# Kernel optimization log

Hardware: AMD Instinct MI355X
Metric: run time of the kernel (lower is better)

## Reference

```python
import jax, jax.numpy as jnp
import numpy as np

N, E, G = 20000, 320000, 128
HID, HEADS, LAYERS, IN = 128, 4, 2, 74
EPS = 1e-5


def setup_inputs() -> dict:
    key = jax.random.key(0)
    ks = jax.random.split(key, 10)
    h = jax.random.normal(ks[0], (N, IN), dtype=jnp.float32)
    src = jax.random.randint(ks[1], (E,), 0, N, dtype=jnp.int32)
    dst = jax.random.randint(ks[2], (E,), 0, N, dtype=jnp.int32)
    graph_ids = jnp.sort(jax.random.randint(ks[3], (N,), 0, G, dtype=jnp.int32))
    W0 = jax.random.normal(ks[4], (HEADS, IN, HID), dtype=jnp.float32) / np.sqrt(IN)
    Wr = jax.random.normal(ks[5], (LAYERS - 1, HEADS, HID, HID), dtype=jnp.float32) / np.sqrt(HID)
    att = jax.random.normal(ks[6], (LAYERS, HEADS, 2 * HID), dtype=jnp.float32) / np.sqrt(2 * HID)
    gamma = jnp.ones((LAYERS, HEADS, HID), dtype=jnp.float32)
    beta = jnp.zeros((LAYERS, HEADS, HID), dtype=jnp.float32)
    out_w = jax.random.normal(ks[7], (LAYERS, HID), dtype=jnp.float32) / np.sqrt(HID)
    out_b = jnp.zeros((LAYERS,), dtype=jnp.float32)
    return {"h": h, "src": src, "dst": dst, "graph_ids": graph_ids,
            "W0": W0, "Wr": Wr, "att": att, "gamma": gamma, "beta": beta,
            "out_w": out_w, "out_b": out_b}


def _gat_head(h, W, a, g, b, src, dst):
    # h: [N, F_in], W: [F_in, HID], a: [2*HID]
    z = h @ W                                  # [N, HID]
    zs, zd = z[src], z[dst]                    # [E, HID] gathers
    e = jax.nn.leaky_relu(zs @ a[:HID] + zd @ a[HID:])  # [E] edge logits
    # segment softmax over incoming edges of each dst node
    emax = jax.ops.segment_max(e, dst, num_segments=N)
    ex = jnp.exp(e - emax[dst])
    denom = jax.ops.segment_sum(ex, dst, num_segments=N)
    alpha = ex / denom[dst]
    hout = jax.ops.segment_sum(alpha[:, None] * zs, dst, num_segments=N)  # [N, HID]
    r = jax.nn.relu(hout)
    # BatchNorm1d (training-mode batch stats, biased variance)
    mean = r.mean(0)
    var = r.var(0)
    return g * (r - mean) / jnp.sqrt(var + EPS) + b


def reference(h, src, dst, graph_ids, W0, Wr, att, gamma, beta, out_w, out_b):
    heads = jax.vmap(_gat_head, in_axes=(None, 0, 0, 0, 0, None, None))
    x = h
    for j in range(LAYERS):
        W = W0 if j == 0 else Wr[j - 1]
        hs = heads(x, W, att[j], gamma[j], beta[j], src, dst)  # [HEADS, N, HID]
        hs = jnp.transpose(hs, (1, 0, 2))                       # [N, HEADS, HID]
        score = jax.nn.softmax(hs @ out_w[j] + out_b[j], axis=1)  # [N, HEADS]
        x = jnp.einsum('nh,nhd->nd', score, hs)                 # [N, HID]
    # dgl.mean_nodes: per-graph mean of node features
    counts = jax.ops.segment_sum(jnp.ones((N,), dtype=x.dtype), graph_ids, num_segments=G)
    sums = jax.ops.segment_sum(x, graph_ids, num_segments=G)
    return sums / jnp.maximum(counts, 1.0)[:, None]
```

## Files before the change

kernel.cpp:

```cpp
#include <hip/hip_runtime.h>
#include <hip/hip_bf16.h>

typedef unsigned short u16;
typedef unsigned int u32;
typedef __attribute__((ext_vector_type(8))) short bf16x8;
typedef __attribute__((ext_vector_type(4))) float f32x4;
typedef __attribute__((ext_vector_type(2))) float f32x2;

#define NN 20000
#define NE 320000
#define NG 128
#define HD 128
#define NH 4
#define KIN 74
#define KP0 96
#define BN_EPS 1e-5f
#define SCAN_B 20

__device__ __forceinline__ float bf2f(u16 v){ return __uint_as_float(((u32)v)<<16); }
__device__ __forceinline__ float bflo(u32 v){ return __uint_as_float(v<<16); }
__device__ __forceinline__ float bfhi(u32 v){ return __uint_as_float(v & 0xffff0000u); }
__device__ __forceinline__ u16 f2bf(float f){
    u32 u = __float_as_uint(f);
    return (u16)((u + 0x7fffu + ((u>>16)&1u)) >> 16);
}
__device__ __forceinline__ u32 pack2(float a, float b){
    return (u32)f2bf(a) | ((u32)f2bf(b) << 16);
}

__global__ void k_hist(const int* __restrict__ dst, int* __restrict__ counts){
    int e = blockIdx.x*256 + threadIdx.x;
    if(e < NE) atomicAdd(&counts[dst[e]], 1);
}

__global__ void k_scan1(const int* __restrict__ counts, int* __restrict__ rowptr,
                        int* __restrict__ tsum){
    __shared__ int wsum[16];
    int tx = threadIdx.x, lane = tx & 63, wid = tx >> 6;
    int i = blockIdx.x*1024 + tx;
    int v = (i < NN) ? counts[i] : 0;
    int s = v;
    #pragma unroll
    for(int d = 1; d < 64; d <<= 1){ int o = __shfl_up(s, d); if(lane >= d) s += o; }
    if(lane == 63) wsum[wid] = s;
    __syncthreads();
    int woff = 0, total = 0;
    #pragma unroll
    for(int w_ = 0; w_ < 16; ++w_){ int sw = wsum[w_]; total += sw; if(w_ < wid) woff += sw; }
    if(i < NN) rowptr[i] = woff + s - v;
    if(tx == 0) tsum[blockIdx.x] = total;
}

__global__ void k_scan2(int* __restrict__ tsum, int* __restrict__ toff,
                        int* __restrict__ rowptr){
    if(threadIdx.x == 0){
        int run = 0;
        for(int b = 0; b < SCAN_B; ++b){ toff[b] = run; run += tsum[b]; }
        rowptr[NN] = run;
    }
}

__global__ void k_scan3(int* __restrict__ rowptr, const int* __restrict__ toff,
                        int* __restrict__ cursor){
    int i = blockIdx.x*1024 + threadIdx.x;
    if(i >= NN) return;
    int v = rowptr[i] + toff[blockIdx.x];
    rowptr[i] = v;
    cursor[i] = v;
}

__global__ void k_scatter(const int* __restrict__ src, const int* __restrict__ dst,
                          int* __restrict__ cursor, int* __restrict__ srcs){
    int e = blockIdx.x*256 + threadIdx.x;
    if(e >= NE) return;
    int d = dst[e];
    int p = atomicAdd(&cursor[d], 1);
    srcs[p] = src[e];
}

__global__ void k_prep_h(const float* __restrict__ h, u16* __restrict__ hb){
    int i = blockIdx.x*256 + threadIdx.x;
    if(i >= NN*KP0) return;
    int n = i / KP0, k = i - n*KP0;
    hb[i] = (k < KIN) ? f2bf(h[n*KIN + k]) : (u16)0;
}

__global__ void k_prep_w0(const float* __restrict__ W0, u16* __restrict__ wt){
    int i = blockIdx.x*256 + threadIdx.x;
    if(i >= NH*HD*KP0) return;
    int k = i % KP0; int c = (i/KP0) % HD; int h = i/(KP0*HD);
    wt[i] = (k < KIN) ? f2bf(W0[(h*KIN + k)*HD + c]) : (u16)0;
}

__global__ void k_prep_w1(const float* __restrict__ Wr, u16* __restrict__ wt){
    int i = blockIdx.x*256 + threadIdx.x;
    if(i >= NH*HD*HD) return;
    int k = i % HD; int c = (i/HD) % HD; int h = i/(HD*HD);
    wt[i] = f2bf(Wr[(h*HD + k)*HD + c]);
}

template<int KP>
__global__ void k_gemm_mfma(const u16* __restrict__ xb, const u16* __restrict__ wt,
                            u16* __restrict__ z){
    int h = blockIdx.y;
    int tx = threadIdx.x, lane = tx & 63, w = tx >> 6;
    int n0 = blockIdx.x*32 + (w >> 1)*16;
    int c0 = (w & 1)*64;
    int r16 = lane & 15, kg = lane >> 4;
    const u16* ap = xb + (size_t)(n0 + r16)*KP + kg*8;
    const u16* bp = wt + ((size_t)h*HD + c0 + r16)*KP + kg*8;
    f32x4 acc0 = {0.f,0.f,0.f,0.f}, acc1 = {0.f,0.f,0.f,0.f};
    f32x4 acc2 = {0.f,0.f,0.f,0.f}, acc3 = {0.f,0.f,0.f,0.f};
    #pragma unroll
    for(int k0 = 0; k0 < KP; k0 += 32){
        bf16x8 av = *(const bf16x8*)(ap + k0);
        bf16x8 b0 = *(const bf16x8*)(bp + k0);
        bf16x8 b1 = *(const bf16x8*)(bp + 16*KP + k0);
        bf16x8 b2 = *(const bf16x8*)(bp + 32*KP + k0);
        bf16x8 b3 = *(const bf16x8*)(bp + 48*KP + k0);
        acc0 = __builtin_amdgcn_mfma_f32_16x16x32_bf16(av, b0, acc0, 0, 0, 0);
        acc1 = __builtin_amdgcn_mfma_f32_16x16x32_bf16(av, b1, acc1, 0, 0, 0);
        acc2 = __builtin_amdgcn_mfma_f32_16x16x32_bf16(av, b2, acc2, 0, 0, 0);
        acc3 = __builtin_amdgcn_mfma_f32_16x16x32_bf16(av, b3, acc3, 0, 0, 0);
    }
    int nbase = n0 + kg*4;
    u16* zp = z + ((size_t)h*NN + nbase)*HD + c0 + r16;
    #pragma unroll
    for(int reg = 0; reg < 4; ++reg){
        u16* q = zp + (size_t)reg*HD;
        q[0]  = f2bf(acc0[reg]);
        q[16] = f2bf(acc1[reg]);
        q[32] = f2bf(acc2[reg]);
        q[48] = f2bf(acc3[reg]);
    }
}

__global__ void k_dots(const u16* __restrict__ z, const float* __restrict__ attj,
                       float* __restrict__ es, float* __restrict__ ed){
    int tx = threadIdx.x, lane = tx & 63, w = tx >> 6;
    int n = blockIdx.x*4 + w;
    int h = blockIdx.y;
    int ch = lane*2;
    u32 zz = *(const u32*)(z + ((size_t)h*NN + n)*HD + ch);
    float z0 = bflo(zz), z1 = bfhi(zz);
    const float* a = attj + h*2*HD;
    float ps = z0*a[ch]    + z1*a[ch+1];
    float pd = z0*a[HD+ch] + z1*a[HD+ch+1];
    #pragma unroll
    for(int d = 32; d > 0; d >>= 1){ ps += __shfl_xor(ps, d); pd += __shfl_xor(pd, d); }
    if(lane == 0){ es[(size_t)h*NN + n] = ps; ed[(size_t)h*NN + n] = pd; }
}

__global__ void k_aggregate(const int* __restrict__ rowptr, const int* __restrict__ srcs,
                            const float* __restrict__ es, const float* __restrict__ ed,
                            const u16* __restrict__ z, u16* __restrict__ r){
    int tx = threadIdx.x, lane = tx & 63, w = tx >> 6;
    int n = blockIdx.x*4 + w;
    int h = blockIdx.y;
    int p0 = rowptr[n], p1 = rowptr[n+1];
    int eslot = lane >> 4;
    int cidx  = lane & 15;
    const float* esh = es + (size_t)h*NN;
    const u16*   zh  = z  + (size_t)h*NN*HD;
    float edn = ed[(size_t)h*NN + n];
    float ssum = 0.f;
    f32x2 acc[4];
    #pragma unroll
    for(int k = 0; k < 4; ++k) acc[k] = (f32x2){0.f, 0.f};

    for(int base = p0; base < p1; base += 64){
        int p = base + lane;
        int sn = 0; float ex = 0.f;
        if(p < p1){
            sn = srcs[p];
            float e = esh[sn] + edn;
            e = e >= 0.f ? e : 0.01f*e;
            ex = __expf(e);
        }
        ssum += ex;
        int cnt = min(64, p1 - base);
        int niter = (cnt + 7) >> 3;
        for(int i = 0; i < niter; ++i){
            int e0 = i*8 + eslot;
            int e1 = e0 + 4;
            float a0 = __shfl(ex, e0);
            int   s0 = __shfl(sn, e0);
            float a1 = __shfl(ex, e1);
            int   s1 = __shfl(sn, e1);
            uint4 v0 = *(const uint4*)(zh + (size_t)s0*HD + cidx*8);
            uint4 v1 = *(const uint4*)(zh + (size_t)s1*HD + cidx*8);
            f32x2 t;
            t.x = bflo(v0.x); t.y = bfhi(v0.x); acc[0] += a0*t;
            t.x = bflo(v0.y); t.y = bfhi(v0.y); acc[1] += a0*t;
            t.x = bflo(v0.z); t.y = bfhi(v0.z); acc[2] += a0*t;
            t.x = bflo(v0.w); t.y = bfhi(v0.w); acc[3] += a0*t;
            t.x = bflo(v1.x); t.y = bfhi(v1.x); acc[0] += a1*t;
            t.x = bflo(v1.y); t.y = bfhi(v1.y); acc[1] += a1*t;
            t.x = bflo(v1.z); t.y = bfhi(v1.z); acc[2] += a1*t;
            t.x = bflo(v1.w); t.y = bfhi(v1.w); acc[3] += a1*t;
        }
    }
    float c01[8];
    #pragma unroll
    for(int k = 0; k < 4; ++k){
        float a0 = acc[k].x, a1 = acc[k].y;
        a0 += __shfl_xor(a0, 16); a0 += __shfl_xor(a0, 32);
        a1 += __shfl_xor(a1, 16); a1 += __shfl_xor(a1, 32);
        c01[k*2] = a0; c01[k*2+1] = a1;
    }
    #pragma unroll
    for(int d = 32; d > 0; d >>= 1) ssum += __shfl_xor(ssum, d);
    float inv = (ssum > 0.f) ? 1.f/ssum : 0.f;
    if(eslot == 0){
        uint4 o;
        o.x = pack2(fmaxf(c01[0]*inv, 0.f), fmaxf(c01[1]*inv, 0.f));
        o.y = pack2(fmaxf(c01[2]*inv, 0.f), fmaxf(c01[3]*inv, 0.f));
        o.z = pack2(fmaxf(c01[4]*inv, 0.f), fmaxf(c01[5]*inv, 0.f));
        o.w = pack2(fmaxf(c01[6]*inv, 0.f), fmaxf(c01[7]*inv, 0.f));
        *(uint4*)(r + ((size_t)n*NH + h)*HD + cidx*8) = o;
    }
}

__global__ void k_bnreduce(const u16* __restrict__ r, float* __restrict__ bnsum,
                           float* __restrict__ bnsqs){
    int c = blockIdx.x*256 + threadIdx.x;
    int nbeg = blockIdx.y * 160;
    float s = 0.f, s2 = 0.f;
    for(int i = 0; i < 160; ++i){
        float v = bf2f(r[(size_t)(nbeg+i)*512 + c]);
        s += v; s2 += v*v;
    }
    atomicAdd(&bnsum[c], s);
    atomicAdd(&bnsqs[c], s2);
}

__global__ void k_bnfin(const float* __restrict__ bnsum, const float* __restrict__ bnsqs,
                        const float* __restrict__ gamma, const float* __restrict__ beta,
                        float* __restrict__ inv, float* __restrict__ shift){
    int c = blockIdx.x*256 + threadIdx.x;
    if(c >= 512) return;
    float mean = bnsum[c] * (1.f/NN);
    float var  = bnsqs[c] * (1.f/NN) - mean*mean;
    float iv = gamma[c] * rsqrtf(var + BN_EPS);
    inv[c] = iv;
    shift[c] = beta[c] - mean*iv;
}

__global__ void k_headmix(const u16* __restrict__ r, const float* __restrict__ inv,
                          const float* __restrict__ shift, const float* __restrict__ ow,
                          u16* __restrict__ x){
    int tx = threadIdx.x, lane = tx & 63, w = tx >> 6;
    int n = blockIdx.x*4 + w;
    if(n >= NN) return;
    int ch = lane*2;
    float rn[NH][2];
    float sc[NH];
    #pragma unroll
    for(int h = 0; h < NH; ++h){
        int c = h*HD + ch;
        u32 zz = *(const u32*)(r + (size_t)n*512 + c);
        float v0 = bflo(zz)*inv[c]   + shift[c];
        float v1 = bfhi(zz)*inv[c+1] + shift[c+1];
        rn[h][0] = v0; rn[h][1] = v1;
        float p = v0*ow[ch] + v1*ow[ch+1];
        #pragma unroll
        for(int d = 32; d > 0; d >>= 1) p += __shfl_xor(p, d);
        sc[h] = p;
    }
    float m = fmaxf(fmaxf(sc[0], sc[1]), fmaxf(sc[2], sc[3]));
    float e0 = __expf(sc[0]-m), e1 = __expf(sc[1]-m), e2 = __expf(sc[2]-m), e3 = __expf(sc[3]-m);
    float is = 1.f/(e0+e1+e2+e3);
    float x0 = (e0*rn[0][0] + e1*rn[1][0] + e2*rn[2][0] + e3*rn[3][0])*is;
    float x1 = (e0*rn[0][1] + e1*rn[1][1] + e2*rn[2][1] + e3*rn[3][1])*is;
    *(u32*)(x + (size_t)n*HD + ch) = pack2(x0, x1);
}

__global__ void k_gmean(const int* __restrict__ gid, const u16* __restrict__ x,
                        float* __restrict__ out){
    int g = blockIdx.x;
    int tx = threadIdx.x, lane = tx & 63, w = tx >> 6;
    int lo = 0, hi = NN;
    while(lo < hi){ int mid = (lo + hi) >> 1; if(gid[mid] < g) lo = mid + 1; else hi = mid; }
    int start = lo;
    hi = NN;
    while(lo < hi){ int mid = (lo + hi) >> 1; if(gid[mid] < g + 1) lo = mid + 1; else hi = mid; }
    int end = lo;
    float a0 = 0.f, a1 = 0.f;
    for(int n = start + w; n < end; n += 4){
        u32 zz = *(const u32*)(x + (size_t)n*HD + lane*2);
        a0 += bflo(zz);
        a1 += bfhi(zz);
    }
    __shared__ float sm[4][HD];
    sm[w][lane*2]     = a0;
    sm[w][lane*2 + 1] = a1;
    __syncthreads();
    if(tx < HD){
        float s = sm[0][tx] + sm[1][tx] + sm[2][tx] + sm[3][tx];
        float cnt = (float)(end - start);
        out[g*HD + tx] = s / fmaxf(cnt, 1.f);
    }
}

extern "C" void kernel_launch(void* const* d_in, const int* in_sizes, int n_in,
                              void* d_out, int out_size, void* d_ws, size_t ws_size,
                              hipStream_t stream){
    const float* h     = (const float*)d_in[0];
    const int*   src   = (const int*)  d_in[1];
    const int*   dst   = (const int*)  d_in[2];
    const int*   gid   = (const int*)  d_in[3];
    const float* W0    = (const float*)d_in[4];
    const float* Wr    = (const float*)d_in[5];
    const float* att   = (const float*)d_in[6];
    const float* gamma = (const float*)d_in[7];
    const float* beta  = (const float*)d_in[8];
    const float* ow    = (const float*)d_in[9];

    char* p = (char*)d_ws;
    auto alloc = [&](size_t bytes) -> void* {
        void* q = (void*)p;
        p += (bytes + 255) & ~(size_t)255;
        return q;
    };
    u16*   z      = (u16*)  alloc((size_t)NN*NH*HD*2);
    u16*   r      = (u16*)  alloc((size_t)NN*NH*HD*2);
    u16*   x      = (u16*)  alloc((size_t)NN*HD*2);
    u16*   hb     = (u16*)  alloc((size_t)NN*KP0*2);
    u16*   wt0    = (u16*)  alloc((size_t)NH*HD*KP0*2);
    u16*   wt1    = (u16*)  alloc((size_t)NH*HD*HD*2);
    float* es     = (float*)alloc((size_t)NN*NH*4);
    float* ed     = (float*)alloc((size_t)NN*NH*4);
    int*   counts = (int*)  alloc((size_t)NN*4);
    int*   rowptr = (int*)  alloc((size_t)(NN+1)*4);
    int*   cursor = (int*)  alloc((size_t)NN*4);
    int*   srcs   = (int*)  alloc((size_t)NE*4);
    int*   tsum   = (int*)  alloc((size_t)SCAN_B*4);
    int*   toff   = (int*)  alloc((size_t)SCAN_B*4);
    float* bnsum  = (float*)alloc(1024*4);
    float* bnsqs  = bnsum + 512;
    float* bninv  = (float*)alloc(1024*4);
    float* bnshift= bninv + 512;

    k_prep_h <<<(NN*KP0+255)/256, 256, 0, stream>>>(h, hb);
    k_prep_w0<<<(NH*HD*KP0+255)/256, 256, 0, stream>>>(W0, wt0);
    k_prep_w1<<<(NH*HD*HD+255)/256, 256, 0, stream>>>(Wr, wt1);

    hipMemsetAsync(counts, 0, (size_t)NN*4, stream);
    k_hist   <<<(NE+255)/256, 256, 0, stream>>>(dst, counts);
    k_scan1  <<<SCAN_B, 1024, 0, stream>>>(counts, rowptr, tsum);
    k_scan2  <<<1, 64, 0, stream>>>(tsum, toff, rowptr);
    k_scan3  <<<SCAN_B, 1024, 0, stream>>>(rowptr, toff, cursor);
    k_scatter<<<(NE+255)/256, 256, 0, stream>>>(src, dst, cursor, srcs);

    for(int j = 0; j < 2; ++j){
        if(j == 0) k_gemm_mfma<KP0><<<dim3(NN/32, NH), 256, 0, stream>>>(hb, wt0, z);
        else       k_gemm_mfma<HD> <<<dim3(NN/32, NH), 256, 0, stream>>>(x,  wt1, z);

        k_dots     <<<dim3(NN/4, NH), 256, 0, stream>>>(z, att + j*NH*2*HD, es, ed);
        k_aggregate<<<dim3(NN/4, NH), 256, 0, stream>>>(rowptr, srcs, es, ed, z, r);

        hipMemsetAsync(bnsum, 0, 1024*4, stream);
        k_bnreduce <<<dim3(2,125), 256, 0, stream>>>(r, bnsum, bnsqs);
        k_bnfin    <<<2, 256, 0, stream>>>(bnsum, bnsqs, gamma + j*512, beta + j*512,
                                           bninv, bnshift);
        k_headmix  <<<NN/4, 256, 0, stream>>>(r, bninv, bnshift, ow + j*HD, x);
    }

    k_gmean<<<NG, 256, 0, stream>>>(gid, x, (float*)d_out);
}
```

Before: 268.5 us.

## Merge prep kernels and memsets, fold scan2 and bnfin into consumers

Combines the three input-conversion kernels and the counts and batch-norm-stat zeroing into one launch. The scan's middle kernel is removed: each block of scan3 now sums the preceding block totals with a wave reduction, and rowptr[NN] is set to NE directly. The BN finalize kernel is folded into headmix, where every block recomputes the 512 scale/shift values into shared memory. The aim is to cut launch count and tiny serial kernels, at the cost of redundant per-block BN finalize work and some branch divergence in the merged prep kernel.

```diff
diff --git a/kernel.cpp b/kernel.cpp
--- a/kernel.cpp
+++ b/kernel.cpp
@@ -28,6 +28,38 @@
     return (u32)f2bf(a) | ((u32)f2bf(b) << 16);
 }
 
+#define PREP_S0 (NN*KP0)
+#define PREP_S1 (NH*HD*KP0)
+#define PREP_S2 (NH*HD*HD)
+#define PREP_TOT (PREP_S0 + PREP_S1 + PREP_S2 + NN + 2048)
+__global__ void k_prep(const float* __restrict__ h, const float* __restrict__ W0,
+                       const float* __restrict__ Wr, u16* __restrict__ hb,
+                       u16* __restrict__ wt0, u16* __restrict__ wt1,
+                       int* __restrict__ counts, float* __restrict__ bnstat){
+    int i = blockIdx.x*256 + threadIdx.x;
+    if(i < PREP_S0){
+        int n = i/KP0, k = i - n*KP0;
+        hb[i] = (k < KIN) ? f2bf(h[n*KIN + k]) : (u16)0;
+        return;
+    }
+    i -= PREP_S0;
+    if(i < PREP_S1){
+        int k = i % KP0; int c = (i/KP0) % HD; int hh = i/(KP0*HD);
+        wt0[i] = (k < KIN) ? f2bf(W0[(hh*KIN + k)*HD + c]) : (u16)0;
+        return;
+    }
+    i -= PREP_S1;
+    if(i < PREP_S2){
+        int k = i % HD; int c = (i/HD) % HD; int hh = i/(HD*HD);
+        wt1[i] = f2bf(Wr[(hh*HD + k)*HD + c]);
+        return;
+    }
+    i -= PREP_S2;
+    if(i < NN){ counts[i] = 0; return; }
+    i -= NN;
+    if(i < 2048) bnstat[i] = 0.f;
+}
+
 __global__ void k_hist(const int* __restrict__ dst, int* __restrict__ counts){
     int e = blockIdx.x*256 + threadIdx.x;
     if(e < NE) atomicAdd(&counts[dst[e]], 1);
@@ -51,22 +83,24 @@
     if(tx == 0) tsum[blockIdx.x] = total;
 }
 
-__global__ void k_scan2(int* __restrict__ tsum, int* __restrict__ toff,
-                        int* __restrict__ rowptr){
-    if(threadIdx.x == 0){
-        int run = 0;
-        for(int b = 0; b < SCAN_B; ++b){ toff[b] = run; run += tsum[b]; }
-        rowptr[NN] = run;
-    }
-}
-
-__global__ void k_scan3(int* __restrict__ rowptr, const int* __restrict__ toff,
+__global__ void k_scan3(int* __restrict__ rowptr, const int* __restrict__ tsum,
                         int* __restrict__ cursor){
-    int i = blockIdx.x*1024 + threadIdx.x;
-    if(i >= NN) return;
-    int v = rowptr[i] + toff[blockIdx.x];
-    rowptr[i] = v;
-    cursor[i] = v;
+    __shared__ int s_off;
+    int tx = threadIdx.x;
+    if(tx < 64){
+        int v = (tx < SCAN_B && tx < (int)blockIdx.x) ? tsum[tx] : 0;
+        #pragma unroll
+        for(int d = 32; d > 0; d >>= 1) v += __shfl_xor(v, d);
+        if(tx == 0) s_off = v;
+    }
+    __syncthreads();
+    int i = blockIdx.x*1024 + tx;
+    if(i < NN){
+        int val = rowptr[i] + s_off;
+        rowptr[i] = val;
+        cursor[i] = val;
+    }
+    if(blockIdx.x == 0 && tx == 0) rowptr[NN] = NE;
 }
 
 __global__ void k_scatter(const int* __restrict__ src, const int* __restrict__ dst,
@@ -76,27 +110,6 @@
     int d = dst[e];
     int p = atomicAdd(&cursor[d], 1);
     srcs[p] = src[e];
-}
-
-__global__ void k_prep_h(const float* __restrict__ h, u16* __restrict__ hb){
-    int i = blockIdx.x*256 + threadIdx.x;
-    if(i >= NN*KP0) return;
-    int n = i / KP0, k = i - n*KP0;
-    hb[i] = (k < KIN) ? f2bf(h[n*KIN + k]) : (u16)0;
-}
-
-__global__ void k_prep_w0(const float* __restrict__ W0, u16* __restrict__ wt){
-    int i = blockIdx.x*256 + threadIdx.x;
-    if(i >= NH*HD*KP0) return;
-    int k = i % KP0; int c = (i/KP0) % HD; int h = i/(KP0*HD);
-    wt[i] = (k < KIN) ? f2bf(W0[(h*KIN + k)*HD + c]) : (u16)0;
-}
-
-__global__ void k_prep_w1(const float* __restrict__ Wr, u16* __restrict__ wt){
-    int i = blockIdx.x*256 + threadIdx.x;
-    if(i >= NH*HD*HD) return;
-    int k = i % HD; int c = (i/HD) % HD; int h = i/(HD*HD);
-    wt[i] = f2bf(Wr[(h*HD + k)*HD + c]);
 }
 
 template<int KP>
@@ -234,24 +247,23 @@
     atomicAdd(&bnsqs[c], s2);
 }
 
-__global__ void k_bnfin(const float* __restrict__ bnsum, const float* __restrict__ bnsqs,
-                        const float* __restrict__ gamma, const float* __restrict__ beta,
-                        float* __restrict__ inv, float* __restrict__ shift){
-    int c = blockIdx.x*256 + threadIdx.x;
-    if(c >= 512) return;
-    float mean = bnsum[c] * (1.f/NN);
-    float var  = bnsqs[c] * (1.f/NN) - mean*mean;
-    float iv = gamma[c] * rsqrtf(var + BN_EPS);
-    inv[c] = iv;
-    shift[c] = beta[c] - mean*iv;
-}
-
-__global__ void k_headmix(const u16* __restrict__ r, const float* __restrict__ inv,
-                          const float* __restrict__ shift, const float* __restrict__ ow,
+__global__ void k_headmix(const u16* __restrict__ r, const float* __restrict__ bnsum,
+                          const float* __restrict__ bnsqs, const float* __restrict__ gamma,
+                          const float* __restrict__ beta, const float* __restrict__ ow,
                           u16* __restrict__ x){
-    int tx = threadIdx.x, lane = tx & 63, w = tx >> 6;
+    __shared__ float sinv[512], sshift[512];
+    int tx = threadIdx.x;
+    #pragma unroll
+    for(int c = tx; c < 512; c += 256){
+        float mean = bnsum[c] * (1.f/NN);
+        float var  = bnsqs[c] * (1.f/NN) - mean*mean;
+        float iv = gamma[c] * rsqrtf(var + BN_EPS);
+        sinv[c] = iv;
+        sshift[c] = beta[c] - mean*iv;
+    }
+    __syncthreads();
+    int lane = tx & 63, w = tx >> 6;
     int n = blockIdx.x*4 + w;
-    if(n >= NN) return;
     int ch = lane*2;
     float rn[NH][2];
     float sc[NH];
@@ -259,8 +271,8 @@
     for(int h = 0; h < NH; ++h){
         int c = h*HD + ch;
         u32 zz = *(const u32*)(r + (size_t)n*512 + c);
-        float v0 = bflo(zz)*inv[c]   + shift[c];
-        float v1 = bfhi(zz)*inv[c+1] + shift[c+1];
+        float v0 = bflo(zz)*sinv[c]   + sshift[c];
+        float v1 = bfhi(zz)*sinv[c+1] + sshift[c+1];
         rn[h][0] = v0; rn[h][1] = v1;
         float p = v0*ow[ch] + v1*ow[ch+1];
         #pragma unroll
@@ -335,35 +347,27 @@
     int*   cursor = (int*)  alloc((size_t)NN*4);
     int*   srcs   = (int*)  alloc((size_t)NE*4);
     int*   tsum   = (int*)  alloc((size_t)SCAN_B*4);
-    int*   toff   = (int*)  alloc((size_t)SCAN_B*4);
-    float* bnsum  = (float*)alloc(1024*4);
-    float* bnsqs  = bnsum + 512;
-    float* bninv  = (float*)alloc(1024*4);
-    float* bnshift= bninv + 512;
-
-    k_prep_h <<<(NN*KP0+255)/256, 256, 0, stream>>>(h, hb);
-    k_prep_w0<<<(NH*HD*KP0+255)/256, 256, 0, stream>>>(W0, wt0);
-    k_prep_w1<<<(NH*HD*HD+255)/256, 256, 0, stream>>>(Wr, wt1);
-
-    hipMemsetAsync(counts, 0, (size_t)NN*4, stream);
+    float* bnstat = (float*)alloc(2048*4);
+
+    k_prep<<<(PREP_TOT+255)/256, 256, 0, stream>>>(h, W0, Wr, hb, wt0, wt1,
+                                                   counts, bnstat);
+
     k_hist   <<<(NE+255)/256, 256, 0, stream>>>(dst, counts);
     k_scan1  <<<SCAN_B, 1024, 0, stream>>>(counts, rowptr, tsum);
-    k_scan2  <<<1, 64, 0, stream>>>(tsum, toff, rowptr);
-    k_scan3  <<<SCAN_B, 1024, 0, stream>>>(rowptr, toff, cursor);
+    k_scan3  <<<SCAN_B, 1024, 0, stream>>>(rowptr, tsum, cursor);
     k_scatter<<<(NE+255)/256, 256, 0, stream>>>(src, dst, cursor, srcs);
 
     for(int j = 0; j < 2; ++j){
+        const float* attj = att + j*NH*2*HD;
         if(j == 0) k_gemm_mfma<KP0><<<dim3(NN/32, NH), 256, 0, stream>>>(hb, wt0, z);
         else       k_gemm_mfma<HD> <<<dim3(NN/32, NH), 256, 0, stream>>>(x,  wt1, z);
 
-        k_dots     <<<dim3(NN/4, NH), 256, 0, stream>>>(z, att + j*NH*2*HD, es, ed);
+        k_dots     <<<dim3(NN/4, NH), 256, 0, stream>>>(z, attj, es, ed);
         k_aggregate<<<dim3(NN/4, NH), 256, 0, stream>>>(rowptr, srcs, es, ed, z, r);
 
-        hipMemsetAsync(bnsum, 0, 1024*4, stream);
-        k_bnreduce <<<dim3(2,125), 256, 0, stream>>>(r, bnsum, bnsqs);
-        k_bnfin    <<<2, 256, 0, stream>>>(bnsum, bnsqs, gamma + j*512, beta + j*512,
-                                           bninv, bnshift);
-        k_headmix  <<<NN/4, 256, 0, stream>>>(r, bninv, bnshift, ow + j*HD, x);
+        k_bnreduce <<<dim3(2,125), 256, 0, stream>>>(r, bnstat + j*1024, bnstat + j*1024 + 512);
+        k_headmix  <<<NN/4, 256, 0, stream>>>(r, bnstat + j*1024, bnstat + j*1024 + 512,
+                                              gamma + j*512, beta + j*512, ow + j*HD, x);
     }
 
     k_gmean<<<NG, 256, 0, stream>>>(gid, x, (float*)d_out);
```

Result: faster. 257.9 us (-4.0%).
